# Kernel optimization log

Measured on AMD Instinct MI355X. Metric: run time of the kernel, lower is better.

Reference implementation:

```python
import jax, jax.numpy as jnp
import numpy as np

N, T, D, H = 128, 64, 1024, 1024
DA = 4  # spatial dim of feature map


def setup_inputs() -> dict:
    key = jax.random.key(0)
    k1, k2, k3, k4, k5 = jax.random.split(key, 5)
    x = jax.random.normal(k1, (N, T, D), dtype=jnp.float32)
    A = jax.random.normal(k2, (N, H, DA, DA), dtype=jnp.float32)
    Wx = jax.random.normal(k3, (D, 4 * H), dtype=jnp.float32) / np.sqrt(D)
    Wh = jax.random.normal(k4, (H, 4 * H), dtype=jnp.float32) / np.sqrt(H)
    Wattn = jax.random.normal(k5, (H, 4 * H), dtype=jnp.float32) / np.sqrt(H)
    b = jnp.zeros((4 * H,), dtype=jnp.float32)
    return {"x": x, "A": A, "Wx": Wx, "Wh": Wh, "Wattn": Wattn, "b": b}


def _dot_product_attention(prev_h, A_flat):
    # prev_h: (N, H), A_flat: (N, H, L) with L = DA*DA
    scores = jnp.einsum('nh,nhl->nl', prev_h, A_flat) / jnp.sqrt(jnp.float32(H))
    w = jax.nn.softmax(scores, axis=-1)              # (N, L)
    attn = jnp.einsum('nhl,nl->nh', A_flat, w)       # (N, H)
    return attn


def reference(x, A, Wx, Wh, Wattn, b):
    A_flat = A.reshape(A.shape[0], A.shape[1], -1)   # (N, H, L)
    h0 = A.mean(axis=(2, 3))                          # (N, H)
    c0 = h0
    x_t = jnp.swapaxes(x, 0, 1)                       # (T, N, D)

    def step(carry, xt):
        h, c = carry
        attn = _dot_product_attention(h, A_flat)
        a = xt @ Wx + h @ Wh + attn @ Wattn + b       # (N, 4H)
        i, f, o, g = jnp.split(a, 4, axis=1)
        i = jax.nn.sigmoid(i)
        f = jax.nn.sigmoid(f)
        o = jax.nn.sigmoid(o)
        g = jnp.tanh(g)
        c_next = f * c + i * g
        h_next = o * jnp.tanh(c_next)
        return (h_next, c_next), h_next

    _, hn = jax.lax.scan(step, (h0, c0), x_t)         # hn: (T, N, H)
    return jnp.swapaxes(hn, 0, 1)                      # (N, T, H)
```

## Files before the change

### kernel.cpp

```cpp
#include <hip/hip_runtime.h>
#include <stdint.h>
#include <math.h>

typedef __attribute__((ext_vector_type(8))) short short8;
typedef __attribute__((ext_vector_type(4))) short short4v;
typedef __attribute__((ext_vector_type(4))) float f32x4;

__device__ __forceinline__ short f2bf(float f){
  union { float f; uint32_t u; } x; x.f = f;
  uint32_t r = x.u + 0x7fffu + ((x.u >> 16) & 1u);
  return (short)(r >> 16);
}
__device__ __forceinline__ float bf2f(short s){
  union { uint32_t u; float f; } x; x.u = ((uint32_t)(uint16_t)s) << 16;
  return x.f;
}

__device__ __forceinline__ unsigned ld_llc_u32(const void* p){
  return __hip_atomic_load((const unsigned*)p, __ATOMIC_RELAXED, __HIP_MEMORY_SCOPE_AGENT);
}
__device__ __forceinline__ void st_llc_u32(void* p, unsigned v){
  __hip_atomic_store((unsigned*)p, v, __ATOMIC_RELAXED, __HIP_MEMORY_SCOPE_AGENT);
}


__global__ __launch_bounds__(256) void k_wt(const float* __restrict__ Wx,
                                            const float* __restrict__ Wh,
                                            const float* __restrict__ Wattn,
                                            short* __restrict__ W3T){
  __shared__ float tile[64][65];
  int bk = blockIdx.x % 48, bj = blockIdx.x / 48;
  int tx = threadIdx.x & 63, ty = threadIdx.x >> 6;
  int k0 = bk * 64, j0 = bj * 64;
  #pragma unroll
  for (int i = 0; i < 16; ++i){
    int kk = ty * 16 + i;
    int k = k0 + kk;
    const float* src = (k < 1024) ? (Wx + (size_t)k * 4096)
                     : (k < 2048) ? (Wh + (size_t)(k - 1024) * 4096)
                                  : (Wattn + (size_t)(k - 2048) * 4096);
    tile[kk][tx] = src[j0 + tx];
  }
  __syncthreads();
  #pragma unroll
  for (int i = 0; i < 16; ++i){
    int jj = ty * 16 + i;
    W3T[(size_t)(j0 + jj) * 3072 + k0 + tx] = f2bf(tile[tx][jj]);
  }
}

__global__ __launch_bounds__(256) void k_cast(const float* __restrict__ in,
                                              short* __restrict__ out, int n4){
  int i = blockIdx.x * 256 + threadIdx.x;
  if (i >= n4) return;
  float4 v = ((const float4*)in)[i];
  short4v o; o[0] = f2bf(v.x); o[1] = f2bf(v.y); o[2] = f2bf(v.z); o[3] = f2bf(v.w);
  *(short4v*)(out + (size_t)i * 4) = o;
}

__global__ __launch_bounds__(256) void k_init(const float* __restrict__ A,
                                              float* __restrict__ c,
                                              short* __restrict__ hb0,
                                              unsigned* __restrict__ flags){
  int idx = blockIdx.x * 256 + threadIdx.x;
  if (idx < 8192) flags[idx] = 0u;
  const float* p = A + (size_t)idx * 16;
  float s = 0.f;
  #pragma unroll
  for (int l = 0; l < 16; ++l) s += p[l];
  s *= (1.f / 16.f);
  c[idx] = s;
  hb0[idx] = f2bf(s);
}

typedef const __attribute__((address_space(1))) uint32_t* gas1_t;
typedef __attribute__((address_space(3))) uint32_t* las3_t;

__global__ __launch_bounds__(256) void k_xwx(const short* __restrict__ xbf,
                                             const short* __restrict__ W3T,
                                             short* __restrict__ xwx){
  __shared__ short ldsA[128 * 64];
  __shared__ short ldsB[128 * 64];
  const int tid  = threadIdx.x;
  const int lane = tid & 63;
  const int wave = tid >> 6;

  const int orig = blockIdx.x;
  const int wg = (orig & 7) * 256 + (orig >> 3);
  const int n_t = wg >> 6;
  const int m_t = wg & 63;
  const int m0 = m_t * 128;
  const int n0 = n_t * 128;

  const int ra = lane & 15;
  const int q  = lane >> 4;

  f32x4 acc[4][4];
  #pragma unroll
  for (int mf = 0; mf < 4; ++mf)
    #pragma unroll
    for (int jf = 0; jf < 4; ++jf) acc[mf][jf] = f32x4{0.f,0.f,0.f,0.f};

  const int wm = wave >> 1;
  const int wn = wave & 1;

  for (int kt = 0; kt < 16; ++kt){
    const int kb = kt * 64;
    #pragma unroll
    for (int r = 0; r < 4; ++r){
      int id = (wave * 4 + r) * 64 + lane;
      int row = id >> 3, c = id & 7;
      int csrc = c ^ (row & 7);
      const short* src = xbf + (size_t)(m0 + row) * 1024 + kb + csrc * 8;
      short* dst = ldsA + (wave * 4 + r) * 512;
      __builtin_amdgcn_global_load_lds((gas1_t)(const void*)src, (las3_t)(void*)dst, 16, 0, 0);
    }
    #pragma unroll
    for (int r = 0; r < 4; ++r){
      int id = (wave * 4 + r) * 64 + lane;
      int row = id >> 3, c = id & 7;
      int csrc = c ^ (row & 7);
      const short* src = W3T + (size_t)(n0 + row) * 3072 + kb + csrc * 8;
      short* dst = ldsB + (wave * 4 + r) * 512;
      __builtin_amdgcn_global_load_lds((gas1_t)(const void*)src, (las3_t)(void*)dst, 16, 0, 0);
    }
    asm volatile("s_waitcnt vmcnt(0)" ::: "memory");
    __syncthreads();

    #pragma unroll
    for (int kk = 0; kk < 64; kk += 32){
      const int cc = (kk >> 3) + q;
      short8 af[4], bfr[4];
      #pragma unroll
      for (int mf = 0; mf < 4; ++mf){
        int row = wm * 64 + mf * 16 + ra;
        af[mf] = *(const short8*)(ldsA + row * 64 + ((cc ^ (row & 7)) << 3));
      }
      #pragma unroll
      for (int jf = 0; jf < 4; ++jf){
        int row = wn * 64 + jf * 16 + ra;
        bfr[jf] = *(const short8*)(ldsB + row * 64 + ((cc ^ (row & 7)) << 3));
      }
      #pragma unroll
      for (int mf = 0; mf < 4; ++mf)
        #pragma unroll
        for (int jf = 0; jf < 4; ++jf)
          acc[mf][jf] = __builtin_amdgcn_mfma_f32_16x16x32_bf16(af[mf], bfr[jf], acc[mf][jf], 0, 0, 0);
    }
    __syncthreads();
  }

  #pragma unroll
  for (int mf = 0; mf < 4; ++mf)
    #pragma unroll
    for (int jf = 0; jf < 4; ++jf)
      #pragma unroll
      for (int i = 0; i < 4; ++i){
        int row = m0 + wm * 64 + mf * 16 + q * 4 + i;
        int col = n0 + wn * 64 + jf * 16 + ra;
        xwx[(size_t)row * 4096 + col] = f2bf(acc[mf][jf][i]);
      }
}

__global__ __launch_bounds__(512, 1) void k_loop(
    const short* __restrict__ W3T,
    const short* __restrict__ Abf,
    short* __restrict__ hbuf,
    short* __restrict__ abuf,
    const float* __restrict__ cbuf,
    const short* __restrict__ xwx,
    const float* __restrict__ bias,
    float* __restrict__ out,
    unsigned* __restrict__ flags)
{
  __shared__ short Wl[65536];
  __shared__ float redu[4096];
  __shared__ float sred[4][16];

  unsigned* flagsB = flags;
  unsigned* flagsA = flags + 4096;
  unsigned* goA    = flags + 6144;
  unsigned* goB    = flags + 6160;

  const int tid  = threadIdx.x;
  const int lane = tid & 63;
  const int wave = tid >> 6;
  const int bid  = blockIdx.x;
  const int mh   = bid & 1;
  const int jb   = bid >> 1;
  const int u0   = jb * 8;
  const int ra   = lane & 15;
  const int q    = lane >> 4;
  const int mf2  = wave & 1;
  const int kh   = wave >> 1;

  #pragma unroll
  for (int it = 0; it < 16; ++it){
    int c16 = it * 512 + tid;
    int jl = c16 >> 8;
    int kc = c16 & 255;
    int jf = jl >> 4, rr = jl & 15;
    int j = (jf * 2 + (rr >> 3)) * 1024 + u0 + (rr & 7);
    short8 v = *(const short8*)(W3T + (size_t)j * 3072 + 1024 + kc * 8);
    int pc = (jf * 16 + rr) * 256 + (kc ^ (rr & 7));
    *(short8*)(Wl + pc * 8) = v;
  }

  short8 af0[4], af1[4];
  const int hh0 = tid * 4;
  if (wave < 4 && bid < 128){
    #pragma unroll
    for (int j = 0; j < 4; ++j){
      const short8* ap = (const short8*)(Abf + ((size_t)bid * 1024 + hh0 + j) * 16);
      af0[j] = ap[0]; af1[j] = ap[1];
    }
  }

  const int n_loc = tid >> 3, uu = tid & 7;
  const int cn = mh * 64 + n_loc;
  const int cu = u0 + uu;
  float creg = cbuf[(size_t)cn * 1024 + cu];
  const float b0 = bias[cu], b1 = bias[1024 + cu], b2 = bias[2048 + cu], b3 = bias[3072 + cu];
  __syncthreads();

  for (int t = 0; t < 64; ++t){
    const short* hRp = hbuf + (size_t)t * 131072;
    short*       hWp = hbuf + (size_t)(t + 1) * 131072;
    short*       aT  = abuf + (size_t)t * 131072;

    if (wave < 4){
      if (t > 0){
        if (bid == 255 && wave == 0){
          for (;;){
            unsigned mn = 0xffffffffu;
            #pragma unroll
            for (int i = 0; i < 4; ++i){
              unsigned v = ld_llc_u32(&flagsB[(lane * 4 + i) * 16]);
              mn = v < mn ? v : mn;
            }
            if (__all(mn >= (unsigned)t)) break;
            __builtin_amdgcn_s_sleep(2);
          }
          if (lane == 0) st_llc_u32(goB, (unsigned)t);
        } else {
          if (lane == 0){
            while (ld_llc_u32(goB) < (unsigned)t) __builtin_amdgcn_s_sleep(1);
          }
        }
        asm volatile("" ::: "memory");
      }
      if (bid < 128){
        uint64_t hq = *(const uint64_t*)(hRp + bid * 1024 + hh0);
        float hv[4];
        #pragma unroll
        for (int j = 0; j < 4; ++j) hv[j] = bf2f((short)((hq >> (16 * j)) & 0xffffu));
        float sc[16];
        #pragma unroll
        for (int l = 0; l < 8; ++l){
          float s0 = 0.f, s1 = 0.f;
          #pragma unroll
          for (int j = 0; j < 4; ++j){ s0 += hv[j] * bf2f(af0[j][l]); s1 += hv[j] * bf2f(af1[j][l]); }
          sc[l] = s0; sc[8 + l] = s1;
        }
        #pragma unroll
        for (int off = 1; off < 64; off <<= 1)
          #pragma unroll
          for (int l = 0; l < 16; ++l) sc[l] += __shfl_xor(sc[l], off);
        if (lane == 0)
          #pragma unroll
          for (int l = 0; l < 16; ++l) sred[wave][l] = sc[l];
      }
    }
    __syncthreads();

    if (wave < 4 && bid < 128){
      float s[16], mx = -1e30f, sum = 0.f;
      #pragma unroll
      for (int l = 0; l < 16; ++l){
        s[l] = (sred[0][l] + sred[1][l] + sred[2][l] + sred[3][l]) * 0.03125f;
        mx = fmaxf(mx, s[l]);
      }
      #pragma unroll
      for (int l = 0; l < 16; ++l){ s[l] = __expf(s[l] - mx); sum += s[l]; }
      const float inv = 1.f / sum;
      unsigned pk[2];
      #pragma unroll
      for (int jp = 0; jp < 2; ++jp){
        float a0 = 0.f, a1 = 0.f;
        #pragma unroll
        for (int l = 0; l < 8; ++l){
          a0 += s[l] * bf2f(af0[jp * 2][l])     + s[8 + l] * bf2f(af1[jp * 2][l]);
          a1 += s[l] * bf2f(af0[jp * 2 + 1][l]) + s[8 + l] * bf2f(af1[jp * 2 + 1][l]);
        }
        pk[jp] = (unsigned)(unsigned short)f2bf(a0 * inv)
               | ((unsigned)(unsigned short)f2bf(a1 * inv) << 16);
      }
      st_llc_u32(aT + bid * 1024 + hh0,     pk[0]);
      st_llc_u32(aT + bid * 1024 + hh0 + 2, pk[1]);
      asm volatile("s_waitcnt vmcnt(0)" ::: "memory");
    }
    __syncthreads();
    if (tid == 0 && bid < 128) st_llc_u32(&flagsA[bid * 16], (unsigned)(t + 1));

    const short* xp = xwx + ((size_t)cn * 64 + t) * 4096;
    const short xw0 = xp[cu], xw1 = xp[1024 + cu], xw2 = xp[2048 + cu], xw3 = xp[3072 + cu];

    auto loadA = [&](int ks, int m) -> short8 {
      const int kk = ks * 32 + q * 8;
      const int row = mh * 64 + mf2 * 32 + m * 16 + ra;
      const short* p = (kh < 2) ? (hRp + row * 1024 + kh * 512 + kk)
                                : (aT + row * 1024 + (kh - 2) * 512 + kk);
      return *(const short8*)p;
    };
    auto loadB = [&](int ks, int jf) -> short8 {
      const int kcg = kh * 64 + ks * 4 + q;
      const int sw = kcg ^ (ra & 7);
      return *(const short8*)(Wl + (((jf * 16 + ra) * 256) + sw) * 8);
    };

    short8 Ab[4][2], Bb[2][2];
    Bb[0][0] = loadB(0, 0); Bb[0][1] = loadB(0, 1);
    Bb[1][0] = loadB(1, 0); Bb[1][1] = loadB(1, 1);

    if (wave < 4){
      #pragma unroll
      for (int p = 0; p < 4; ++p){ Ab[p][0] = loadA(p, 0); Ab[p][1] = loadA(p, 1); }
    } else {
      if (bid == 255 && wave == 4){
        for (;;){
          unsigned mn = 0xffffffffu;
          unsigned v0 = ld_llc_u32(&flagsA[(lane * 2) * 16]);
          unsigned v1 = ld_llc_u32(&flagsA[(lane * 2 + 1) * 16]);
          mn = v0 < v1 ? v0 : v1;
          if (__all(mn >= (unsigned)(t + 1))) break;
          __builtin_amdgcn_s_sleep(2);
        }
        if (lane == 0) st_llc_u32(goA, (unsigned)(t + 1));
      } else {
        if (lane == 0){
          while (ld_llc_u32(goA) < (unsigned)(t + 1)) __builtin_amdgcn_s_sleep(1);
        }
      }
      asm volatile("" ::: "memory");
      #pragma unroll
      for (int p = 0; p < 4; ++p){ Ab[p][0] = loadA(p, 0); Ab[p][1] = loadA(p, 1); }
    }

    f32x4 acc[2][2];
    acc[0][0] = f32x4{0.f,0.f,0.f,0.f}; acc[0][1] = f32x4{0.f,0.f,0.f,0.f};
    acc[1][0] = f32x4{0.f,0.f,0.f,0.f}; acc[1][1] = f32x4{0.f,0.f,0.f,0.f};

    #pragma unroll
    for (int ks = 0; ks < 16; ++ks){
      short8 av0 = Ab[ks & 3][0], av1 = Ab[ks & 3][1];
      short8 bv0 = Bb[ks & 1][0], bv1 = Bb[ks & 1][1];
      if (ks < 12){ Ab[ks & 3][0] = loadA(ks + 4, 0); Ab[ks & 3][1] = loadA(ks + 4, 1); }
      if (ks < 14){ Bb[ks & 1][0] = loadB(ks + 2, 0); Bb[ks & 1][1] = loadB(ks + 2, 1); }
      acc[0][0] = __builtin_amdgcn_mfma_f32_16x16x32_bf16(av0, bv0, acc[0][0], 0, 0, 0);
      acc[0][1] = __builtin_amdgcn_mfma_f32_16x16x32_bf16(av0, bv1, acc[0][1], 0, 0, 0);
      acc[1][0] = __builtin_amdgcn_mfma_f32_16x16x32_bf16(av1, bv0, acc[1][0], 0, 0, 0);
      acc[1][1] = __builtin_amdgcn_mfma_f32_16x16x32_bf16(av1, bv1, acc[1][1], 0, 0, 0);
    }

    auto ridx = [&](int m2, int khq, int m, int jf) -> float* {
      return &redu[((((m2 * 2 + khq) * 2 + m) * 2 + jf) * 64 + lane) * 4];
    };
    if (kh & 1){
      *(f32x4*)ridx(mf2, kh >> 1, 0, 0) = acc[0][0];
      *(f32x4*)ridx(mf2, kh >> 1, 0, 1) = acc[0][1];
      *(f32x4*)ridx(mf2, kh >> 1, 1, 0) = acc[1][0];
      *(f32x4*)ridx(mf2, kh >> 1, 1, 1) = acc[1][1];
    }
    __syncthreads();
    if (!(kh & 1)){
      acc[0][0] += *(const f32x4*)ridx(mf2, kh >> 1, 0, 0);
      acc[0][1] += *(const f32x4*)ridx(mf2, kh >> 1, 0, 1);
      acc[1][0] += *(const f32x4*)ridx(mf2, kh >> 1, 1, 0);
      acc[1][1] += *(const f32x4*)ridx(mf2, kh >> 1, 1, 1);
    }
    __syncthreads();
    if (kh == 2){
      *(f32x4*)ridx(mf2, 0, 0, 0) = acc[0][0];
      *(f32x4*)ridx(mf2, 0, 0, 1) = acc[0][1];
      *(f32x4*)ridx(mf2, 0, 1, 0) = acc[1][0];
      *(f32x4*)ridx(mf2, 0, 1, 1) = acc[1][1];
    }
    __syncthreads();
    if (kh == 0){
      acc[0][0] += *(const f32x4*)ridx(mf2, 0, 0, 0);
      acc[0][1] += *(const f32x4*)ridx(mf2, 0, 0, 1);
      acc[1][0] += *(const f32x4*)ridx(mf2, 0, 1, 0);
      acc[1][1] += *(const f32x4*)ridx(mf2, 0, 1, 1);
    }
    __syncthreads();
    if (kh == 0){
      #pragma unroll
      for (int m = 0; m < 2; ++m)
        #pragma unroll
        for (int jf = 0; jf < 2; ++jf){
          const int g = jf * 2 + (ra >> 3);
          const int nl = mf2 * 32 + m * 16 + q * 4;
          #pragma unroll
          for (int i = 0; i < 4; ++i)
            redu[g * 512 + (nl + i) * 8 + (ra & 7)] = acc[m][jf][i];
        }
    }
    __syncthreads();

    float hn;
    {
      const float av = redu[tid]        + bf2f(xw0) + b0;
      const float fv = redu[512 + tid]  + bf2f(xw1) + b1;
      const float ov = redu[1024 + tid] + bf2f(xw2) + b2;
      const float gv = redu[1536 + tid] + bf2f(xw3) + b3;
      const float ig = 1.f / (1.f + __expf(-av));
      const float fg = 1.f / (1.f + __expf(-fv));
      const float og = 1.f / (1.f + __expf(-ov));
      const float gcl = fminf(fmaxf(gv, -20.f), 20.f);
      const float e2g = __expf(2.f * gcl);
      const float gg = (e2g - 1.f) / (e2g + 1.f);
      creg = fg * creg + ig * gg;
      const float ccl = fminf(fmaxf(creg, -20.f), 20.f);
      const float e2c = __expf(2.f * ccl);
      const float th = (e2c - 1.f) / (e2c + 1.f);
      hn = og * th;
      const float hn2 = __shfl_xor(hn, 1);
      if ((tid & 1) == 0){
        unsigned pk = (unsigned)(unsigned short)f2bf(hn)
                    | ((unsigned)(unsigned short)f2bf(hn2) << 16);
        st_llc_u32(hWp + (size_t)cn * 1024 + cu, pk);
      }
    }
    asm volatile("s_waitcnt vmcnt(0)" ::: "memory");
    __syncthreads();
    if (tid == 0 && t < 63) st_llc_u32(&flagsB[bid * 16], (unsigned)(t + 1));
    __builtin_nontemporal_store(hn, &out[((size_t)cn * 64 + t) * 1024 + cu]);
  }
}


extern "C" void kernel_launch(void* const* d_in, const int* in_sizes, int n_in,
                              void* d_out, int out_size, void* d_ws, size_t ws_size,
                              hipStream_t stream)
{
  const float* x     = (const float*)d_in[0];
  const float* A     = (const float*)d_in[1];
  const float* Wx    = (const float*)d_in[2];
  const float* Wh    = (const float*)d_in[3];
  const float* Wattn = (const float*)d_in[4];
  const float* b     = (const float*)d_in[5];
  float* out = (float*)d_out;
  char* ws = (char*)d_ws;

  short*    W3T   = (short*)(ws + 0);
  short*    Abf   = (short*)(ws + 25165824);
  short*    xbf   = (short*)(ws + 29360128);
  short*    xwx   = (short*)(ws + 46137344);
  short*    hbuf  = (short*)(ws + 113246208);
  short*    abuf  = (short*)(ws + 130285568);
  float*    cbuf  = (float*)(ws + 147062784);
  unsigned* flags = (unsigned*)(ws + 147587072);

  hipLaunchKernelGGL(k_wt,   dim3(48 * 64), dim3(256), 0, stream, Wx, Wh, Wattn, W3T);
  hipLaunchKernelGGL(k_cast, dim3(2097152 / 256), dim3(256), 0, stream, x, xbf, 2097152);
  hipLaunchKernelGGL(k_cast, dim3(524288 / 256),  dim3(256), 0, stream, A, Abf, 524288);
  hipLaunchKernelGGL(k_init, dim3(512), dim3(256), 0, stream, A, cbuf, hbuf, flags);
  hipLaunchKernelGGL(k_xwx,  dim3(2048), dim3(256), 0, stream, xbf, W3T, xwx);
  hipLaunchKernelGGL(k_loop, dim3(256), dim3(512), 0, stream,
                     W3T, Abf, hbuf, abuf, cbuf, xwx, b, out, flags);
}
```

Baseline: 936.4 us.

## Precompute A·Wattn per batch so recurrent GEMM only multiplies h by Wh

Measured after the change: 892.8 us. 1.05x faster.

```diff
diff --git a/kernel.cpp b/kernel.cpp
--- a/kernel.cpp
+++ b/kernel.cpp
@@ -58,6 +58,41 @@
   *(short4v*)(out + (size_t)i * 4) = o;
 }
 
+__global__ __launch_bounds__(256) void k_castA(const float* __restrict__ A,
+                                               short* __restrict__ Abf,
+                                               short* __restrict__ Atr){
+  const int n = blockIdx.x;
+  const int tid = threadIdx.x;
+  __shared__ short tile[256][17];
+  for (int it = 0; it < 4; ++it){
+    int h = it * 256 + tid;
+    const float* src = A + ((size_t)n * 1024 + h) * 16;
+    short o[16];
+    #pragma unroll
+    for (int l = 0; l < 16; ++l) o[l] = f2bf(src[l]);
+    short8 p0, p1;
+    #pragma unroll
+    for (int l = 0; l < 8; ++l){ p0[l] = o[l]; p1[l] = o[8 + l]; }
+    short8* dst = (short8*)(Abf + ((size_t)n * 1024 + h) * 16);
+    dst[0] = p0; dst[1] = p1;
+    #pragma unroll
+    for (int l = 0; l < 16; ++l) tile[tid][l] = o[l];
+    __syncthreads();
+    {
+      int l = tid >> 4, hc = (tid & 15) * 16;
+      short tmp[16];
+      #pragma unroll
+      for (int k = 0; k < 16; ++k) tmp[k] = tile[hc + k][l];
+      short8 q0, q1;
+      #pragma unroll
+      for (int k = 0; k < 8; ++k){ q0[k] = tmp[k]; q1[k] = tmp[8 + k]; }
+      short8* d2 = (short8*)(Atr + (size_t)n * 16384 + l * 1024 + it * 256 + hc);
+      d2[0] = q0; d2[1] = q1;
+    }
+    __syncthreads();
+  }
+}
+
 __global__ __launch_bounds__(256) void k_init(const float* __restrict__ A,
                                               float* __restrict__ c,
                                               short* __restrict__ hb0,
@@ -84,14 +119,12 @@
   const int tid  = threadIdx.x;
   const int lane = tid & 63;
   const int wave = tid >> 6;
-
   const int orig = blockIdx.x;
   const int wg = (orig & 7) * 256 + (orig >> 3);
   const int n_t = wg >> 6;
   const int m_t = wg & 63;
   const int m0 = m_t * 128;
   const int n0 = n_t * 128;
-
   const int ra = lane & 15;
   const int q  = lane >> 4;
 
@@ -162,25 +195,78 @@
       }
 }
 
+__global__ __launch_bounds__(256) void k_pw(const short* __restrict__ W3T,
+                                            const short* __restrict__ Atr,
+                                            short* __restrict__ P){
+  const int tid  = threadIdx.x;
+  const int lane = tid & 63;
+  const int wave = tid >> 6;
+  const int blk  = blockIdx.x;
+  const int n    = blk >> 4;
+  const int jblk = blk & 15;
+  const int j0   = jblk * 256 + wave * 64;
+  const int ra = lane & 15;
+  const int q  = lane >> 4;
+
+  f32x4 acc[4];
+  #pragma unroll
+  for (int mf = 0; mf < 4; ++mf) acc[mf] = f32x4{0.f,0.f,0.f,0.f};
+
+  auto loadA = [&](int ks, int mf) -> short8 {
+    return *(const short8*)(W3T + (size_t)(j0 + mf*16 + ra) * 3072 + 2048 + ks * 32 + q * 8);
+  };
+  auto loadB = [&](int ks) -> short8 {
+    return *(const short8*)(Atr + (size_t)n * 16384 + ra * 1024 + ks * 32 + q * 8);
+  };
+
+  short8 aC[4], bC, aN[4], bN;
+  #pragma unroll
+  for (int mf = 0; mf < 4; ++mf) aC[mf] = loadA(0, mf);
+  bC = loadB(0);
+  for (int ks = 0; ks < 32; ++ks){
+    bool more = (ks + 1) < 32;
+    if (more){
+      #pragma unroll
+      for (int mf = 0; mf < 4; ++mf) aN[mf] = loadA(ks + 1, mf);
+      bN = loadB(ks + 1);
+    }
+    #pragma unroll
+    for (int mf = 0; mf < 4; ++mf)
+      acc[mf] = __builtin_amdgcn_mfma_f32_16x16x32_bf16(aC[mf], bC, acc[mf], 0, 0, 0);
+    if (more){
+      #pragma unroll
+      for (int mf = 0; mf < 4; ++mf) aC[mf] = aN[mf];
+      bC = bN;
+    }
+  }
+  #pragma unroll
+  for (int mf = 0; mf < 4; ++mf)
+    #pragma unroll
+    for (int i = 0; i < 4; ++i){
+      int j = j0 + mf * 16 + q * 4 + i;
+      P[(size_t)(n * 4096 + j) * 16 + ra] = f2bf(acc[mf][i]);
+    }
+}
+
 __global__ __launch_bounds__(512, 1) void k_loop(
     const short* __restrict__ W3T,
     const short* __restrict__ Abf,
+    const short* __restrict__ P,
     short* __restrict__ hbuf,
-    short* __restrict__ abuf,
+    float* __restrict__ wbuf,
     const float* __restrict__ cbuf,
     const short* __restrict__ xwx,
     const float* __restrict__ bias,
     float* __restrict__ out,
     unsigned* __restrict__ flags)
 {
-  __shared__ short Wl[65536];
+  __shared__ short Wl[32768];
   __shared__ float redu[4096];
   __shared__ float sred[4][16];
+  __shared__ float wlds[64][16];
 
   unsigned* flagsB = flags;
-  unsigned* flagsA = flags + 4096;
-  unsigned* goA    = flags + 6144;
-  unsigned* goB    = flags + 6160;
+  unsigned* wtag   = flags + 4096;
 
   const int tid  = threadIdx.x;
   const int lane = tid & 63;
@@ -193,25 +279,27 @@
   const int q    = lane >> 4;
   const int mf2  = wave & 1;
   const int kh   = wave >> 1;
-
-  #pragma unroll
-  for (int it = 0; it < 16; ++it){
+  const bool isScore = (bid < 128);
+  const int n_s  = mh * 64 + jb;
+
+  #pragma unroll
+  for (int it = 0; it < 8; ++it){
     int c16 = it * 512 + tid;
-    int jl = c16 >> 8;
-    int kc = c16 & 255;
+    int jl = c16 >> 7;
+    int kc = c16 & 127;
     int jf = jl >> 4, rr = jl & 15;
     int j = (jf * 2 + (rr >> 3)) * 1024 + u0 + (rr & 7);
     short8 v = *(const short8*)(W3T + (size_t)j * 3072 + 1024 + kc * 8);
-    int pc = (jf * 16 + rr) * 256 + (kc ^ (rr & 7));
+    int pc = (jf * 16 + rr) * 128 + (kc ^ (rr & 7));
     *(short8*)(Wl + pc * 8) = v;
   }
 
   short8 af0[4], af1[4];
   const int hh0 = tid * 4;
-  if (wave < 4 && bid < 128){
+  if (wave < 4 && isScore){
     #pragma unroll
     for (int j = 0; j < 4; ++j){
-      const short8* ap = (const short8*)(Abf + ((size_t)bid * 1024 + hh0 + j) * 16);
+      const short8* ap = (const short8*)(Abf + ((size_t)n_s * 1024 + hh0 + j) * 16);
       af0[j] = ap[0]; af1[j] = ap[1];
     }
   }
@@ -226,54 +314,43 @@
   for (int t = 0; t < 64; ++t){
     const short* hRp = hbuf + (size_t)t * 131072;
     short*       hWp = hbuf + (size_t)(t + 1) * 131072;
-    short*       aT  = abuf + (size_t)t * 131072;
-
-    if (wave < 4){
-      if (t > 0){
-        if (bid == 255 && wave == 0){
-          for (;;){
-            unsigned mn = 0xffffffffu;
-            #pragma unroll
-            for (int i = 0; i < 4; ++i){
-              unsigned v = ld_llc_u32(&flagsB[(lane * 4 + i) * 16]);
-              mn = v < mn ? v : mn;
-            }
-            if (__all(mn >= (unsigned)t)) break;
-            __builtin_amdgcn_s_sleep(2);
-          }
-          if (lane == 0) st_llc_u32(goB, (unsigned)t);
-        } else {
-          if (lane == 0){
-            while (ld_llc_u32(goB) < (unsigned)t) __builtin_amdgcn_s_sleep(1);
-          }
-        }
-        asm volatile("" ::: "memory");
-      }
-      if (bid < 128){
-        uint64_t hq = *(const uint64_t*)(hRp + bid * 1024 + hh0);
-        float hv[4];
+    float*       wT  = wbuf + (size_t)t * 4096;
+
+    if (t > 0){
+      const unsigned tgt = (unsigned)t;
+      for (;;){
+        unsigned v0 = ld_llc_u32(&flagsB[(mh * 128 + lane * 2)     * 16]);
+        unsigned v1 = ld_llc_u32(&flagsB[(mh * 128 + lane * 2 + 1) * 16]);
+        unsigned mn = v0 < v1 ? v0 : v1;
+        if (__all(mn >= tgt)) break;
+        __builtin_amdgcn_s_sleep(1);
+      }
+    }
+
+    if (wave < 4 && isScore){
+      uint64_t hq = *(const uint64_t*)(hRp + n_s * 1024 + hh0);
+      float hv[4];
+      #pragma unroll
+      for (int j = 0; j < 4; ++j) hv[j] = bf2f((short)((hq >> (16 * j)) & 0xffffu));
+      float sc[16];
+      #pragma unroll
+      for (int l = 0; l < 8; ++l){
+        float s0 = 0.f, s1 = 0.f;
         #pragma unroll
-        for (int j = 0; j < 4; ++j) hv[j] = bf2f((short)((hq >> (16 * j)) & 0xffffu));
-        float sc[16];
+        for (int j = 0; j < 4; ++j){ s0 += hv[j] * bf2f(af0[j][l]); s1 += hv[j] * bf2f(af1[j][l]); }
+        sc[l] = s0; sc[8 + l] = s1;
+      }
+      #pragma unroll
+      for (int off = 1; off < 64; off <<= 1)
         #pragma unroll
-        for (int l = 0; l < 8; ++l){
-          float s0 = 0.f, s1 = 0.f;
-          #pragma unroll
-          for (int j = 0; j < 4; ++j){ s0 += hv[j] * bf2f(af0[j][l]); s1 += hv[j] * bf2f(af1[j][l]); }
-          sc[l] = s0; sc[8 + l] = s1;
-        }
+        for (int l = 0; l < 16; ++l) sc[l] += __shfl_xor(sc[l], off);
+      if (lane == 0)
         #pragma unroll
-        for (int off = 1; off < 64; off <<= 1)
-          #pragma unroll
-          for (int l = 0; l < 16; ++l) sc[l] += __shfl_xor(sc[l], off);
-        if (lane == 0)
-          #pragma unroll
-          for (int l = 0; l < 16; ++l) sred[wave][l] = sc[l];
-      }
-    }
-    __syncthreads();
-
-    if (wave < 4 && bid < 128){
+        for (int l = 0; l < 16; ++l) sred[wave][l] = sc[l];
+    }
+    __syncthreads();
+
+    if (wave == 0 && isScore){
       float s[16], mx = -1e30f, sum = 0.f;
       #pragma unroll
       for (int l = 0; l < 16; ++l){
@@ -283,79 +360,47 @@
       #pragma unroll
       for (int l = 0; l < 16; ++l){ s[l] = __expf(s[l] - mx); sum += s[l]; }
       const float inv = 1.f / sum;
-      unsigned pk[2];
-      #pragma unroll
-      for (int jp = 0; jp < 2; ++jp){
-        float a0 = 0.f, a1 = 0.f;
-        #pragma unroll
-        for (int l = 0; l < 8; ++l){
-          a0 += s[l] * bf2f(af0[jp * 2][l])     + s[8 + l] * bf2f(af1[jp * 2][l]);
-          a1 += s[l] * bf2f(af0[jp * 2 + 1][l]) + s[8 + l] * bf2f(af1[jp * 2 + 1][l]);
+      #pragma unroll
+      for (int l = 0; l < 16; ++l){
+        if (lane == l){
+          union { float f; unsigned u; } cv; cv.f = s[l] * inv;
+          st_llc_u32(&wT[n_s * 32 + l], cv.u);
         }
-        pk[jp] = (unsigned)(unsigned short)f2bf(a0 * inv)
-               | ((unsigned)(unsigned short)f2bf(a1 * inv) << 16);
-      }
-      st_llc_u32(aT + bid * 1024 + hh0,     pk[0]);
-      st_llc_u32(aT + bid * 1024 + hh0 + 2, pk[1]);
+      }
       asm volatile("s_waitcnt vmcnt(0)" ::: "memory");
-    }
-    __syncthreads();
-    if (tid == 0 && bid < 128) st_llc_u32(&flagsA[bid * 16], (unsigned)(t + 1));
+      if (lane == 0) st_llc_u32(&wtag[n_s * 16], (unsigned)(t + 1));
+    }
 
     const short* xp = xwx + ((size_t)cn * 64 + t) * 4096;
     const short xw0 = xp[cu], xw1 = xp[1024 + cu], xw2 = xp[2048 + cu], xw3 = xp[3072 + cu];
 
     auto loadA = [&](int ks, int m) -> short8 {
-      const int kk = ks * 32 + q * 8;
+      const int kk = kh * 256 + ks * 32 + q * 8;
       const int row = mh * 64 + mf2 * 32 + m * 16 + ra;
-      const short* p = (kh < 2) ? (hRp + row * 1024 + kh * 512 + kk)
-                                : (aT + row * 1024 + (kh - 2) * 512 + kk);
-      return *(const short8*)p;
+      return *(const short8*)(hRp + row * 1024 + kk);
     };
     auto loadB = [&](int ks, int jf) -> short8 {
-      const int kcg = kh * 64 + ks * 4 + q;
+      const int kcg = kh * 32 + ks * 4 + q;
       const int sw = kcg ^ (ra & 7);
-      return *(const short8*)(Wl + (((jf * 16 + ra) * 256) + sw) * 8);
+      return *(const short8*)(Wl + (((jf * 16 + ra) * 128) + sw) * 8);
     };
 
     short8 Ab[4][2], Bb[2][2];
     Bb[0][0] = loadB(0, 0); Bb[0][1] = loadB(0, 1);
     Bb[1][0] = loadB(1, 0); Bb[1][1] = loadB(1, 1);
-
-    if (wave < 4){
-      #pragma unroll
-      for (int p = 0; p < 4; ++p){ Ab[p][0] = loadA(p, 0); Ab[p][1] = loadA(p, 1); }
-    } else {
-      if (bid == 255 && wave == 4){
-        for (;;){
-          unsigned mn = 0xffffffffu;
-          unsigned v0 = ld_llc_u32(&flagsA[(lane * 2) * 16]);
-          unsigned v1 = ld_llc_u32(&flagsA[(lane * 2 + 1) * 16]);
-          mn = v0 < v1 ? v0 : v1;
-          if (__all(mn >= (unsigned)(t + 1))) break;
-          __builtin_amdgcn_s_sleep(2);
-        }
-        if (lane == 0) st_llc_u32(goA, (unsigned)(t + 1));
-      } else {
-        if (lane == 0){
-          while (ld_llc_u32(goA) < (unsigned)(t + 1)) __builtin_amdgcn_s_sleep(1);
-        }
-      }
-      asm volatile("" ::: "memory");
-      #pragma unroll
-      for (int p = 0; p < 4; ++p){ Ab[p][0] = loadA(p, 0); Ab[p][1] = loadA(p, 1); }
-    }
+    #pragma unroll
+    for (int p = 0; p < 4; ++p){ Ab[p][0] = loadA(p, 0); Ab[p][1] = loadA(p, 1); }
 
     f32x4 acc[2][2];
     acc[0][0] = f32x4{0.f,0.f,0.f,0.f}; acc[0][1] = f32x4{0.f,0.f,0.f,0.f};
     acc[1][0] = f32x4{0.f,0.f,0.f,0.f}; acc[1][1] = f32x4{0.f,0.f,0.f,0.f};
 
     #pragma unroll
-    for (int ks = 0; ks < 16; ++ks){
+    for (int ks = 0; ks < 8; ++ks){
       short8 av0 = Ab[ks & 3][0], av1 = Ab[ks & 3][1];
       short8 bv0 = Bb[ks & 1][0], bv1 = Bb[ks & 1][1];
-      if (ks < 12){ Ab[ks & 3][0] = loadA(ks + 4, 0); Ab[ks & 3][1] = loadA(ks + 4, 1); }
-      if (ks < 14){ Bb[ks & 1][0] = loadB(ks + 2, 0); Bb[ks & 1][1] = loadB(ks + 2, 1); }
+      if (ks < 4){ Ab[ks & 3][0] = loadA(ks + 4, 0); Ab[ks & 3][1] = loadA(ks + 4, 1); }
+      if (ks < 6){ Bb[ks & 1][0] = loadB(ks + 2, 0); Bb[ks & 1][1] = loadB(ks + 2, 1); }
       acc[0][0] = __builtin_amdgcn_mfma_f32_16x16x32_bf16(av0, bv0, acc[0][0], 0, 0, 0);
       acc[0][1] = __builtin_amdgcn_mfma_f32_16x16x32_bf16(av0, bv1, acc[0][1], 0, 0, 0);
       acc[1][0] = __builtin_amdgcn_mfma_f32_16x16x32_bf16(av1, bv0, acc[1][0], 0, 0, 0);
@@ -377,6 +422,18 @@
       acc[0][1] += *(const f32x4*)ridx(mf2, kh >> 1, 0, 1);
       acc[1][0] += *(const f32x4*)ridx(mf2, kh >> 1, 1, 0);
       acc[1][1] += *(const f32x4*)ridx(mf2, kh >> 1, 1, 1);
+    }
+    if (wave == 2){
+      const unsigned tgt = (unsigned)(t + 1);
+      for (;;){
+        unsigned v = ld_llc_u32(&wtag[(mh * 64 + lane) * 16]);
+        if (__all(v >= tgt)) break;
+        __builtin_amdgcn_s_sleep(1);
+      }
+      const f32x4* wp = (const f32x4*)(wT + (mh * 64 + lane) * 32);
+      f32x4 w0 = wp[0], w1 = wp[1], w2 = wp[2], w3 = wp[3];
+      f32x4* wd = (f32x4*)&wlds[lane][0];
+      wd[0] = w0; wd[1] = w1; wd[2] = w2; wd[3] = w3;
     }
     __syncthreads();
     if (kh == 2){
@@ -409,10 +466,23 @@
 
     float hn;
     {
-      const float av = redu[tid]        + bf2f(xw0) + b0;
-      const float fv = redu[512 + tid]  + bf2f(xw1) + b1;
-      const float ov = redu[1024 + tid] + bf2f(xw2) + b2;
-      const float gv = redu[1536 + tid] + bf2f(xw3) + b3;
+      float wl[16];
+      #pragma unroll
+      for (int l = 0; l < 16; ++l) wl[l] = wlds[n_loc][l];
+      float pg[4];
+      #pragma unroll
+      for (int g = 0; g < 4; ++g){
+        const short8* pp = (const short8*)(P + ((size_t)cn * 4096 + g * 1024 + cu) * 16);
+        short8 pa = pp[0], pb = pp[1];
+        float s = 0.f;
+        #pragma unroll
+        for (int l = 0; l < 8; ++l){ s += bf2f(pa[l]) * wl[l]; s += bf2f(pb[l]) * wl[8 + l]; }
+        pg[g] = s;
+      }
+      const float av = redu[tid]        + bf2f(xw0) + pg[0] + b0;
+      const float fv = redu[512 + tid]  + bf2f(xw1) + pg[1] + b1;
+      const float ov = redu[1024 + tid] + bf2f(xw2) + pg[2] + b2;
+      const float gv = redu[1536 + tid] + bf2f(xw3) + pg[3] + b3;
       const float ig = 1.f / (1.f + __expf(-av));
       const float fg = 1.f / (1.f + __expf(-fv));
       const float og = 1.f / (1.f + __expf(-ov));
@@ -433,7 +503,7 @@
     }
     asm volatile("s_waitcnt vmcnt(0)" ::: "memory");
     __syncthreads();
-    if (tid == 0 && t < 63) st_llc_u32(&flagsB[bid * 16], (unsigned)(t + 1));
+    if (tid == 0 && t < 63) st_llc_u32(&flagsB[(mh * 128 + jb) * 16], (unsigned)(t + 1));
     __builtin_nontemporal_store(hn, &out[((size_t)cn * 64 + t) * 1024 + cu]);
   }
 }
@@ -454,18 +524,21 @@
 
   short*    W3T   = (short*)(ws + 0);
   short*    Abf   = (short*)(ws + 25165824);
-  short*    xbf   = (short*)(ws + 29360128);
-  short*    xwx   = (short*)(ws + 46137344);
-  short*    hbuf  = (short*)(ws + 113246208);
-  short*    abuf  = (short*)(ws + 130285568);
-  float*    cbuf  = (float*)(ws + 147062784);
-  unsigned* flags = (unsigned*)(ws + 147587072);
-
-  hipLaunchKernelGGL(k_wt,   dim3(48 * 64), dim3(256), 0, stream, Wx, Wh, Wattn, W3T);
-  hipLaunchKernelGGL(k_cast, dim3(2097152 / 256), dim3(256), 0, stream, x, xbf, 2097152);
-  hipLaunchKernelGGL(k_cast, dim3(524288 / 256),  dim3(256), 0, stream, A, Abf, 524288);
-  hipLaunchKernelGGL(k_init, dim3(512), dim3(256), 0, stream, A, cbuf, hbuf, flags);
-  hipLaunchKernelGGL(k_xwx,  dim3(2048), dim3(256), 0, stream, xbf, W3T, xwx);
-  hipLaunchKernelGGL(k_loop, dim3(256), dim3(512), 0, stream,
-                     W3T, Abf, hbuf, abuf, cbuf, xwx, b, out, flags);
-}
+  short*    Atr   = (short*)(ws + 29360128);
+  short*    xbf   = (short*)(ws + 33554432);
+  short*    xwx   = (short*)(ws + 50331648);
+  short*    P     = (short*)(ws + 117440512);
+  short*    hbuf  = (short*)(ws + 134217728);
+  float*    wbuf  = (float*)(ws + 151257088);
+  float*    cbuf  = (float*)(ws + 152305664);
+  unsigned* flags = (unsigned*)(ws + 152829952);
+
+  hipLaunchKernelGGL(k_wt,    dim3(48 * 64), dim3(256), 0, stream, Wx, Wh, Wattn, W3T);
+  hipLaunchKernelGGL(k_cast,  dim3(2097152 / 256), dim3(256), 0, stream, x, xbf, 2097152);
+  hipLaunchKernelGGL(k_castA, dim3(128), dim3(256), 0, stream, A, Abf, Atr);
+  hipLaunchKernelGGL(k_init,  dim3(512), dim3(256), 0, stream, A, cbuf, hbuf, flags);
+  hipLaunchKernelGGL(k_xwx,   dim3(2048), dim3(256), 0, stream, xbf, W3T, xwx);
+  hipLaunchKernelGGL(k_pw,    dim3(2048), dim3(256), 0, stream, W3T, Atr, P);
+  hipLaunchKernelGGL(k_loop,  dim3(256), dim3(512), 0, stream,
+                     W3T, Abf, P, hbuf, wbuf, cbuf, xwx, b, out, flags);
+}
```
